# Performance work log

Hardware: AMD Instinct MI355X
Metric: run time of the kernel (lower is better)

## Reference

```python
import jax, jax.numpy as jnp
import numpy as np

D = 8        # input_path_dim (number of driving channels / base vector fields)
N = 256      # cde_state_dim
H = 512      # vf_hidden_dim
B = 4096     # batch of evaluation points (vmapped calls)
P = D * (D - 1) // 2            # number of depth-2 Lyndon brackets (i<j)
M = D + P                       # total brackets = depth-2 Lyndon basis size
_II, _JJ = np.triu_indices(D, k=1)   # Lyndon words (i,j), i<j


def _mlp_fields(h, W1, b1, W2, b2, W3, b3, Wo, bo):
    # eqx.nn.MLP(in=N, out=D*N, width=H, depth=3, softplus hidden, tanh final)
    x = jax.nn.softplus(W1 @ h + b1)
    x = jax.nn.softplus(W2 @ x + b2)
    x = jax.nn.softplus(W3 @ x + b3)
    return jnp.tanh(Wo @ x + bo).reshape(D, N)   # V_i(h), i=1..D


def setup_inputs() -> dict:
    key = jax.random.key(0)
    ks = jax.random.split(key, 10)

    def lin(kw, kb, out_dim, in_dim):
        lim = 1.0 / np.sqrt(in_dim)
        W = jax.random.uniform(kw, (out_dim, in_dim), minval=-lim, maxval=lim, dtype=jnp.float32)
        b = jax.random.uniform(kb, (out_dim,), minval=-lim, maxval=lim, dtype=jnp.float32)
        return W, b

    W1, b1 = lin(ks[0], ks[1], H, N)
    W2, b2 = lin(ks[2], ks[3], H, H)
    W3, b3 = lin(ks[4], ks[5], H, H)
    Wo, bo = lin(ks[6], ks[7], D * N, H)
    h = jax.random.normal(ks[8], (B, N), dtype=jnp.float32)
    primitive_signature = jax.random.normal(ks[9], (B, M), dtype=jnp.float32) * 0.1
    return {
        "h": h, "primitive_signature": primitive_signature,
        "W1": W1, "b1": b1, "W2": W2, "b2": b2,
        "W3": W3, "b3": b3, "Wo": Wo, "bo": bo,
    }


def reference(h, primitive_signature, W1, b1, W2, b2, W3, b3, Wo, bo):
    def single(hv, sig):
        F = lambda y: _mlp_fields(y, W1, b1, W2, b2, W3, b3, Wo, bo)  # [D, N]
        V = F(hv)                                                      # level-1 brackets V_i(h)
        # J[k, i] = DV_i(h) @ V_k(h); one jvp per base-field direction
        J = jax.vmap(lambda v: jax.jvp(F, (hv,), (v,))[1])(V)          # [D, D, N]
        # Lyndon lift, depth 2: [V_i, V_j](h) = DV_j V_i - DV_i V_j, i<j
        lvl2 = J[_II, _JJ] - J[_JJ, _II]                               # [P, N]
        brackets = jnp.concatenate([V, lvl2], axis=0)                  # [M, N]
        # log-ODE contraction against primitive log-signature coefficients
        return jnp.einsum("mn,m->n", brackets, sig)                    # [N]

    return jax.vmap(single)(h, primitive_signature)                    # [B, N]
```

## Files before the change

kernel.cpp:

```cpp
#include <hip/hip_runtime.h>
#include <hip/hip_bf16.h>
#include <math.h>

#define MM 36

typedef _Float16 f16;
typedef __attribute__((ext_vector_type(8))) _Float16 f16x8;
typedef __attribute__((ext_vector_type(4))) _Float16 f16x4;
typedef __attribute__((ext_vector_type(4))) float f32x4;

enum { EPI_NONE = 0, EPI_SPSIG = 1, EPI_TANH = 2, EPI_GATE = 3 };

__device__ __forceinline__ void gl_lds16(const f16* g, f16* l) {
    __builtin_amdgcn_global_load_lds(
        (const __attribute__((address_space(1))) void*)g,
        (__attribute__((address_space(3))) void*)l, 16, 0, 0);
}

template <int EPI, int BM>
__global__ __launch_bounds__(256, 3) void gemm16(
    const f16* __restrict__ A, int lda, long aZ,
    const f16* __restrict__ W, int ldw, long wZ,
    const float* __restrict__ bias,
    void* __restrict__ C0v, int ldc, long cZ,
    f16* __restrict__ C1,
    const f16* __restrict__ G,
    int K, int cshift)
{
    constexpr int WCOLS = (BM == 128) ? 2 : 4;
    constexpr int FN    = (BM == 128) ? 4 : 2;

    __shared__ f16 As[2][BM * 32];
    __shared__ f16 Ws[2][128 * 32];

    const int t = threadIdx.x;
    const int z = blockIdx.z;
    A += (size_t)z * aZ;
    W += (size_t)z * wZ;

    const int nxy = gridDim.x * gridDim.y;
    const int orig = blockIdx.x + gridDim.x * blockIdx.y;
    const int q = nxy >> 3, r = nxy & 7;
    const int xcd = orig & 7, idx = orig >> 3;
    const int nid = (xcd < r ? xcd * (q + 1) : r * (q + 1) + (xcd - r) * q) + idx;
    const long rowTile = (long)(nid >> cshift) * BM;
    const long colTile = (long)(nid & ((1 << cshift) - 1)) * 128;

    const int wave = t >> 6;
    const int lane = t & 63;
    const int wr = (wave / WCOLS) * 64;
    const int wc = (wave % WCOLS) * (FN * 16);
    const int lr = lane & 15;
    const int lk = lane >> 4;

    const int srow = t >> 2;
    const int skq = (t & 3) * 8;
    const f16* Ag = A + (rowTile + srow) * lda + skq;
    const f16* Wg = W + (colTile + srow) * ldw + skq;
    const long lda64 = (long)lda * 64;
    const long ldw64 = (long)ldw * 64;

    f32x4 acc[4][FN];
    const f32x4 zero = {0.f, 0.f, 0.f, 0.f};
#pragma unroll
    for (int m = 0; m < 4; ++m)
#pragma unroll
        for (int n = 0; n < FN; ++n) acc[m][n] = zero;

    const int nt = K >> 5;
    gl_lds16(Ag, &As[0][t * 8]);
    if constexpr (BM == 128) gl_lds16(Ag + lda64, &As[0][(t + 256) * 8]);
    gl_lds16(Wg, &Ws[0][t * 8]);
    gl_lds16(Wg + ldw64, &Ws[0][(t + 256) * 8]);

    for (int ti = 0; ti < nt; ++ti) {
        const int buf = ti & 1;
        __syncthreads();
        if (ti + 1 < nt) {
            const int k0 = (ti + 1) << 5;
            gl_lds16(Ag + k0, &As[buf ^ 1][t * 8]);
            if constexpr (BM == 128) gl_lds16(Ag + k0 + lda64, &As[buf ^ 1][(t + 256) * 8]);
            gl_lds16(Wg + k0, &Ws[buf ^ 1][t * 8]);
            gl_lds16(Wg + k0 + ldw64, &Ws[buf ^ 1][(t + 256) * 8]);
        }
        f16x8 a[4], b[FN];
#pragma unroll
        for (int m = 0; m < 4; ++m)
            a[m] = *(const f16x8*)&As[buf][(wr + m * 16 + lr) * 32 + lk * 8];
#pragma unroll
        for (int n = 0; n < FN; ++n)
            b[n] = *(const f16x8*)&Ws[buf][(wc + n * 16 + lr) * 32 + lk * 8];
#pragma unroll
        for (int m = 0; m < 4; ++m)
#pragma unroll
            for (int n = 0; n < FN; ++n)
                acc[m][n] = __builtin_amdgcn_mfma_f32_16x16x32_f16(a[m], b[n], acc[m][n], 0, 0, 0);
    }

    const long row0 = rowTile + wr + lk * 4;
    const long col0 = colTile + wc + lr;

#pragma unroll
    for (int m = 0; m < 4; ++m) {
#pragma unroll
        for (int n = 0; n < FN; ++n) {
            const long col = col0 + n * 16;
            const float bb = bias ? bias[col] : 0.f;
#pragma unroll
            for (int j = 0; j < 4; ++j) {
                const long row = row0 + m * 16 + j;
                const float x = acc[m][n][j] + bb;
                if constexpr (EPI == EPI_SPSIG) {
                    const float e = __expf(-fabsf(x));
                    const float r1 = __builtin_amdgcn_rcpf(1.f + e);
                    const float sp = fmaxf(x, 0.f) + __logf(1.f + e);
                    const float sg = (x >= 0.f) ? r1 : e * r1;
                    f16* S = (f16*)C0v;
                    S[row * ldc + col] = (f16)sp;
                    C1[row * ldc + col] = (f16)sg;
                } else if constexpr (EPI == EPI_TANH) {
                    const float e2 = __expf(2.f * x);
                    const float th = 1.f - 2.f * __builtin_amdgcn_rcpf(e2 + 1.f);
                    f16* S = (f16*)C0v;
                    S[row * ldc + col] = (f16)th;
                } else if constexpr (EPI == EPI_GATE) {
                    f16* S = (f16*)C0v;
                    const float g = (float)G[(row >> 3) * ldc + col];
                    S[row * ldc + col] = (f16)(x * g);
                } else {
                    float* S = (float*)C0v + (size_t)z * cZ;
                    S[row * ldc + col] = x;
                }
            }
        }
    }
}

__global__ __launch_bounds__(256) void ktilde16(
    const f16* __restrict__ V, const float* __restrict__ sig,
    f16* __restrict__ T, int b0)
{
    const int bl = blockIdx.x * 4 + (threadIdx.x >> 6);
    const int n0 = (threadIdx.x & 63) * 4;
    const f16* vb = V + (size_t)bl * 2048 + n0;
    float v[8][4];
#pragma unroll
    for (int k = 0; k < 8; ++k) {
        const f16x4 x = *(const f16x4*)&vb[k * 256];
#pragma unroll
        for (int j = 0; j < 4; ++j) v[k][j] = (float)x[j];
    }
    const float* sg = sig + (size_t)(b0 + bl) * MM + 8;
    float s2[28];
#pragma unroll
    for (int p = 0; p < 28; ++p) s2[p] = sg[p];

    f16* tb = T + (size_t)bl * 2048 + n0;
#pragma unroll
    for (int i = 0; i < 8; ++i) {
        float a0 = 0.f, a1 = 0.f, a2 = 0.f, a3 = 0.f;
#pragma unroll
        for (int k = 0; k < 8; ++k) {
            if (k == i) continue;
            const int a = (k < i) ? k : i;
            const int b = (k < i) ? i : k;
            const int p = a * (15 - a) / 2 + (b - a - 1);
            const float c = (k < i) ? s2[p] : -s2[p];
            a0 = fmaf(c, v[k][0], a0); a1 = fmaf(c, v[k][1], a1);
            a2 = fmaf(c, v[k][2], a2); a3 = fmaf(c, v[k][3], a3);
        }
        f16x4 o;
        o[0] = (f16)a0; o[1] = (f16)a1; o[2] = (f16)a2; o[3] = (f16)a3;
        *(f16x4*)&tb[i * 256] = o;
    }
}

__global__ __launch_bounds__(256) void finish16(
    const f16* __restrict__ V, const float* __restrict__ Oi,
    const float* __restrict__ sig, float* __restrict__ out, int b0, int C)
{
    const int bl = blockIdx.x * 4 + (threadIdx.x >> 6);
    const int n0 = (threadIdx.x & 63) * 4;
    const float* sg = sig + (size_t)(b0 + bl) * MM;
    float a0 = 0.f, a1 = 0.f, a2 = 0.f, a3 = 0.f;
#pragma unroll
    for (int i = 0; i < 8; ++i) {
        const f16x4 vv = *(const f16x4*)&V[(size_t)bl * 2048 + i * 256 + n0];
        const float4 o = *(const float4*)&Oi[((size_t)i * C + bl) * 256 + n0];
        const float s = sg[i];
        const float v0 = (float)vv[0], v1 = (float)vv[1];
        const float v2 = (float)vv[2], v3 = (float)vv[3];
        a0 = fmaf(s, v0, a0); a0 = fmaf(1.f - v0 * v0, o.x, a0);
        a1 = fmaf(s, v1, a1); a1 = fmaf(1.f - v1 * v1, o.y, a1);
        a2 = fmaf(s, v2, a2); a2 = fmaf(1.f - v2 * v2, o.z, a2);
        a3 = fmaf(s, v3, a3); a3 = fmaf(1.f - v3 * v3, o.w, a3);
    }
    float4 ov; ov.x = a0; ov.y = a1; ov.z = a2; ov.w = a3;
    *(float4*)&out[(size_t)(b0 + bl) * 256 + n0] = ov;
}

__global__ __launch_bounds__(256) void cvt16(
    const float* __restrict__ x, f16* __restrict__ y, int n)
{
    const int i = (blockIdx.x * 256 + threadIdx.x) * 4;
    if (i < n) {
        const float4 v = *(const float4*)&x[i];
        f16x4 o;
        o[0] = (f16)v.x; o[1] = (f16)v.y; o[2] = (f16)v.z; o[3] = (f16)v.w;
        *(f16x4*)&y[i] = o;
    }
}

extern "C" void kernel_launch(void* const* d_in, const int* in_sizes, int n_in,
                              void* d_out, int out_size, void* d_ws, size_t ws_size,
                              hipStream_t stream) {
    const float* h   = (const float*)d_in[0];
    const float* sig = (const float*)d_in[1];
    const float* W1  = (const float*)d_in[2];
    const float* b1  = (const float*)d_in[3];
    const float* W2  = (const float*)d_in[4];
    const float* b2  = (const float*)d_in[5];
    const float* W3  = (const float*)d_in[6];
    const float* b3  = (const float*)d_in[7];
    const float* Wo  = (const float*)d_in[8];
    const float* bo  = (const float*)d_in[9];
    float* out = (float*)d_out;

    char* p = (char*)d_ws;
    f16* W1h = (f16*)p; p += (size_t)512 * 256 * 2;
    f16* W2h = (f16*)p; p += (size_t)512 * 512 * 2;
    f16* W3h = (f16*)p; p += (size_t)512 * 512 * 2;
    f16* Woh = (f16*)p; p += (size_t)2048 * 512 * 2;
    const size_t fixed = (size_t)(p - (char*)d_ws);

    int C = 4096;
    while (C > 128 && fixed + (size_t)C * 31232 > ws_size) C >>= 1;

    f16* h16 = (f16*)p; p += (size_t)C * 256 * 2;
    f16* s1 = (f16*)p;  p += (size_t)C * 512 * 2;
    f16* g1 = (f16*)p;  p += (size_t)C * 512 * 2;
    f16* s2 = (f16*)p;  p += (size_t)C * 512 * 2;
    f16* g2 = (f16*)p;  p += (size_t)C * 512 * 2;
    f16* s3 = (f16*)p;  p += (size_t)C * 512 * 2;
    f16* g3 = (f16*)p;  p += (size_t)C * 512 * 2;
    f16* V  = (f16*)p;  p += (size_t)C * 2048 * 2;
    f16* T  = (f16*)p;  p += (size_t)C * 2048 * 2;
    f16* Ua = (f16*)p;  p += (size_t)C * 4096 * 2;
    f16* Ub = (f16*)p;
    float* Oi = (float*)Ub;

    const dim3 blk(256);
    cvt16<<<dim3(512 * 256 / 1024), blk, 0, stream>>>(W1, W1h, 512 * 256);
    cvt16<<<dim3(512 * 512 / 1024), blk, 0, stream>>>(W2, W2h, 512 * 512);
    cvt16<<<dim3(512 * 512 / 1024), blk, 0, stream>>>(W3, W3h, 512 * 512);
    cvt16<<<dim3(2048 * 512 / 1024), blk, 0, stream>>>(Wo, Woh, 2048 * 512);

    for (int b0 = 0; b0 < 4096; b0 += C) {
        cvt16<<<dim3(C * 256 / 1024), blk, 0, stream>>>(h + (size_t)b0 * 256, h16, C * 256);
        gemm16<EPI_SPSIG, 64><<<dim3(4, C / 64), blk, 0, stream>>>(
            h16, 256, 0, W1h, 256, 0, b1, s1, 512, 0, g1, nullptr, 256, 2);
        gemm16<EPI_SPSIG, 64><<<dim3(4, C / 64), blk, 0, stream>>>(
            s1, 512, 0, W2h, 512, 0, b2, s2, 512, 0, g2, nullptr, 512, 2);
        gemm16<EPI_SPSIG, 64><<<dim3(4, C / 64), blk, 0, stream>>>(
            s2, 512, 0, W3h, 512, 0, b3, s3, 512, 0, g3, nullptr, 512, 2);
        gemm16<EPI_TANH, 128><<<dim3(16, C / 128), blk, 0, stream>>>(
            s3, 512, 0, Woh, 512, 0, bo, V, 2048, 0, nullptr, nullptr, 512, 4);
        ktilde16<<<dim3(C / 4), blk, 0, stream>>>(V, sig, T, b0);
        gemm16<EPI_GATE, 128><<<dim3(4, C / 16), blk, 0, stream>>>(
            T, 256, 0, W1h, 256, 0, nullptr, Ua, 512, 0, nullptr, g1, 256, 2);
        gemm16<EPI_GATE, 128><<<dim3(4, C / 16), blk, 0, stream>>>(
            Ua, 512, 0, W2h, 512, 0, nullptr, Ub, 512, 0, nullptr, g2, 512, 2);
        gemm16<EPI_GATE, 128><<<dim3(4, C / 16), blk, 0, stream>>>(
            Ub, 512, 0, W3h, 512, 0, nullptr, Ua, 512, 0, nullptr, g3, 512, 2);
        gemm16<EPI_NONE, 128><<<dim3(2, C / 128, 8), blk, 0, stream>>>(
            Ua, 4096, 512, Woh, 512, (long)256 * 512, nullptr, Oi, 256, (long)C * 256,
            nullptr, nullptr, 512, 1);
        finish16<<<dim3(C / 4), blk, 0, stream>>>(V, Oi, sig, out, b0, C);
    }
}
```

Measured before the change: 186.5 us.

## Generalize GEMM tiling, use 512-thread 256-row tiles, fp16 Oi, fuse weight casts

Templates the GEMM on tile sizes, thread count and wave layout, and switches the output and tangent GEMMs to 256x128 tiles run by 512 threads. The goal is more operand reuse per staged tile. The final per-channel GEMM now stores its result in fp16 instead of fp32, which halves that traffic but costs some precision. The four weight-conversion launches are merged into one kernel. The larger tiles need more LDS and registers per block, which may limit occupancy.

```diff
diff --git a/kernel.cpp b/kernel.cpp
--- a/kernel.cpp
+++ b/kernel.cpp
@@ -17,8 +17,8 @@
         (__attribute__((address_space(3))) void*)l, 16, 0, 0);
 }
 
-template <int EPI, int BM>
-__global__ __launch_bounds__(256, 3) void gemm16(
+template <int EPI, int BM, int BN, int TPB, int WN>
+__global__ __launch_bounds__(TPB, (TPB == 512) ? 6 : 3) void gemm16(
     const f16* __restrict__ A, int lda, long aZ,
     const f16* __restrict__ W, int ldw, long wZ,
     const float* __restrict__ bias,
@@ -27,11 +27,14 @@
     const f16* __restrict__ G,
     int K, int cshift)
 {
-    constexpr int WCOLS = (BM == 128) ? 2 : 4;
-    constexpr int FN    = (BM == 128) ? 4 : 2;
+    constexpr int WM = TPB / 64 / WN;
+    constexpr int FM = BM / (WM * 16);
+    constexpr int FN = BN / (WN * 16);
+    constexpr int LA = BM * 4 / TPB;
+    constexpr int LB = BN * 4 / TPB;
 
     __shared__ f16 As[2][BM * 32];
-    __shared__ f16 Ws[2][128 * 32];
+    __shared__ f16 Ws[2][BN * 32];
 
     const int t = threadIdx.x;
     const int z = blockIdx.z;
@@ -44,54 +47,51 @@
     const int xcd = orig & 7, idx = orig >> 3;
     const int nid = (xcd < r ? xcd * (q + 1) : r * (q + 1) + (xcd - r) * q) + idx;
     const long rowTile = (long)(nid >> cshift) * BM;
-    const long colTile = (long)(nid & ((1 << cshift) - 1)) * 128;
+    const long colTile = (long)(nid & ((1 << cshift) - 1)) * BN;
 
     const int wave = t >> 6;
     const int lane = t & 63;
-    const int wr = (wave / WCOLS) * 64;
-    const int wc = (wave % WCOLS) * (FN * 16);
+    const int wr = (wave / WN) * (FM * 16);
+    const int wc = (wave % WN) * (FN * 16);
     const int lr = lane & 15;
     const int lk = lane >> 4;
 
-    const int srow = t >> 2;
-    const int skq = (t & 3) * 8;
-    const f16* Ag = A + (rowTile + srow) * lda + skq;
-    const f16* Wg = W + (colTile + srow) * ldw + skq;
-    const long lda64 = (long)lda * 64;
-    const long ldw64 = (long)ldw * 64;
-
-    f32x4 acc[4][FN];
+    const f16* Ag = A + (rowTile + (t >> 2)) * lda + (t & 3) * 8;
+    const f16* Wg = W + (colTile + (t >> 2)) * ldw + (t & 3) * 8;
+
+    f32x4 acc[FM][FN];
     const f32x4 zero = {0.f, 0.f, 0.f, 0.f};
 #pragma unroll
-    for (int m = 0; m < 4; ++m)
+    for (int m = 0; m < FM; ++m)
 #pragma unroll
         for (int n = 0; n < FN; ++n) acc[m][n] = zero;
 
     const int nt = K >> 5;
-    gl_lds16(Ag, &As[0][t * 8]);
-    if constexpr (BM == 128) gl_lds16(Ag + lda64, &As[0][(t + 256) * 8]);
-    gl_lds16(Wg, &Ws[0][t * 8]);
-    gl_lds16(Wg + ldw64, &Ws[0][(t + 256) * 8]);
+
+    auto stage = [&](int buf, int k0) {
+#pragma unroll
+        for (int p = 0; p < LA; ++p)
+            gl_lds16(Ag + (long)p * (TPB / 4) * lda + k0, &As[buf][(p * TPB + t) * 8]);
+#pragma unroll
+        for (int p = 0; p < LB; ++p)
+            gl_lds16(Wg + (long)p * (TPB / 4) * ldw + k0, &Ws[buf][(p * TPB + t) * 8]);
+    };
+
+    stage(0, 0);
 
     for (int ti = 0; ti < nt; ++ti) {
         const int buf = ti & 1;
         __syncthreads();
-        if (ti + 1 < nt) {
-            const int k0 = (ti + 1) << 5;
-            gl_lds16(Ag + k0, &As[buf ^ 1][t * 8]);
-            if constexpr (BM == 128) gl_lds16(Ag + k0 + lda64, &As[buf ^ 1][(t + 256) * 8]);
-            gl_lds16(Wg + k0, &Ws[buf ^ 1][t * 8]);
-            gl_lds16(Wg + k0 + ldw64, &Ws[buf ^ 1][(t + 256) * 8]);
-        }
-        f16x8 a[4], b[FN];
-#pragma unroll
-        for (int m = 0; m < 4; ++m)
+        if (ti + 1 < nt) stage(buf ^ 1, (ti + 1) << 5);
+        f16x8 a[FM], b[FN];
+#pragma unroll
+        for (int m = 0; m < FM; ++m)
             a[m] = *(const f16x8*)&As[buf][(wr + m * 16 + lr) * 32 + lk * 8];
 #pragma unroll
         for (int n = 0; n < FN; ++n)
             b[n] = *(const f16x8*)&Ws[buf][(wc + n * 16 + lr) * 32 + lk * 8];
 #pragma unroll
-        for (int m = 0; m < 4; ++m)
+        for (int m = 0; m < FM; ++m)
 #pragma unroll
             for (int n = 0; n < FN; ++n)
                 acc[m][n] = __builtin_amdgcn_mfma_f32_16x16x32_f16(a[m], b[n], acc[m][n], 0, 0, 0);
@@ -101,7 +101,7 @@
     const long col0 = colTile + wc + lr;
 
 #pragma unroll
-    for (int m = 0; m < 4; ++m) {
+    for (int m = 0; m < FM; ++m) {
 #pragma unroll
         for (int n = 0; n < FN; ++n) {
             const long col = col0 + n * 16;
@@ -128,8 +128,8 @@
                     const float g = (float)G[(row >> 3) * ldc + col];
                     S[row * ldc + col] = (f16)(x * g);
                 } else {
-                    float* S = (float*)C0v + (size_t)z * cZ;
-                    S[row * ldc + col] = x;
+                    f16* S = (f16*)C0v + (size_t)z * cZ;
+                    S[row * ldc + col] = (f16)x;
                 }
             }
         }
@@ -176,7 +176,7 @@
 }
 
 __global__ __launch_bounds__(256) void finish16(
-    const f16* __restrict__ V, const float* __restrict__ Oi,
+    const f16* __restrict__ V, const f16* __restrict__ Oi,
     const float* __restrict__ sig, float* __restrict__ out, int b0, int C)
 {
     const int bl = blockIdx.x * 4 + (threadIdx.x >> 6);
@@ -186,17 +186,36 @@
 #pragma unroll
     for (int i = 0; i < 8; ++i) {
         const f16x4 vv = *(const f16x4*)&V[(size_t)bl * 2048 + i * 256 + n0];
-        const float4 o = *(const float4*)&Oi[((size_t)i * C + bl) * 256 + n0];
+        const f16x4 oo = *(const f16x4*)&Oi[((size_t)i * C + bl) * 256 + n0];
         const float s = sg[i];
         const float v0 = (float)vv[0], v1 = (float)vv[1];
         const float v2 = (float)vv[2], v3 = (float)vv[3];
-        a0 = fmaf(s, v0, a0); a0 = fmaf(1.f - v0 * v0, o.x, a0);
-        a1 = fmaf(s, v1, a1); a1 = fmaf(1.f - v1 * v1, o.y, a1);
-        a2 = fmaf(s, v2, a2); a2 = fmaf(1.f - v2 * v2, o.z, a2);
-        a3 = fmaf(s, v3, a3); a3 = fmaf(1.f - v3 * v3, o.w, a3);
+        a0 = fmaf(s, v0, a0); a0 = fmaf(1.f - v0 * v0, (float)oo[0], a0);
+        a1 = fmaf(s, v1, a1); a1 = fmaf(1.f - v1 * v1, (float)oo[1], a1);
+        a2 = fmaf(s, v2, a2); a2 = fmaf(1.f - v2 * v2, (float)oo[2], a2);
+        a3 = fmaf(s, v3, a3); a3 = fmaf(1.f - v3 * v3, (float)oo[3], a3);
     }
     float4 ov; ov.x = a0; ov.y = a1; ov.z = a2; ov.w = a3;
     *(float4*)&out[(size_t)(b0 + bl) * 256 + n0] = ov;
+}
+
+__global__ __launch_bounds__(256) void cvtW(
+    const float* __restrict__ W1, const float* __restrict__ W2,
+    const float* __restrict__ W3, const float* __restrict__ Wo,
+    f16* __restrict__ o1, f16* __restrict__ o2,
+    f16* __restrict__ o3, f16* __restrict__ oo)
+{
+    long i = (long)blockIdx.x * 256 + threadIdx.x;
+    const float* src; f16* dst; long base;
+    if (i < 32768)       { src = W1; dst = o1; base = 0; }
+    else if (i < 98304)  { src = W2; dst = o2; base = 32768; }
+    else if (i < 163840) { src = W3; dst = o3; base = 98304; }
+    else                 { src = Wo; dst = oo; base = 163840; }
+    i -= base;
+    const float4 v = ((const float4*)src)[i];
+    f16x4 o;
+    o[0] = (f16)v.x; o[1] = (f16)v.y; o[2] = (f16)v.z; o[3] = (f16)v.w;
+    ((f16x4*)dst)[i] = o;
 }
 
 __global__ __launch_bounds__(256) void cvt16(
@@ -247,32 +266,30 @@
     f16* T  = (f16*)p;  p += (size_t)C * 2048 * 2;
     f16* Ua = (f16*)p;  p += (size_t)C * 4096 * 2;
     f16* Ub = (f16*)p;
-    float* Oi = (float*)Ub;
+    f16* Oi = Ub;
 
     const dim3 blk(256);
-    cvt16<<<dim3(512 * 256 / 1024), blk, 0, stream>>>(W1, W1h, 512 * 256);
-    cvt16<<<dim3(512 * 512 / 1024), blk, 0, stream>>>(W2, W2h, 512 * 512);
-    cvt16<<<dim3(512 * 512 / 1024), blk, 0, stream>>>(W3, W3h, 512 * 512);
-    cvt16<<<dim3(2048 * 512 / 1024), blk, 0, stream>>>(Wo, Woh, 2048 * 512);
+    const dim3 blk5(512);
+    cvtW<<<dim3(1664), blk, 0, stream>>>(W1, W2, W3, Wo, W1h, W2h, W3h, Woh);
 
     for (int b0 = 0; b0 < 4096; b0 += C) {
         cvt16<<<dim3(C * 256 / 1024), blk, 0, stream>>>(h + (size_t)b0 * 256, h16, C * 256);
-        gemm16<EPI_SPSIG, 64><<<dim3(4, C / 64), blk, 0, stream>>>(
+        gemm16<EPI_SPSIG, 64, 128, 256, 4><<<dim3(4, C / 64), blk, 0, stream>>>(
             h16, 256, 0, W1h, 256, 0, b1, s1, 512, 0, g1, nullptr, 256, 2);
-        gemm16<EPI_SPSIG, 64><<<dim3(4, C / 64), blk, 0, stream>>>(
+        gemm16<EPI_SPSIG, 64, 128, 256, 4><<<dim3(4, C / 64), blk, 0, stream>>>(
             s1, 512, 0, W2h, 512, 0, b2, s2, 512, 0, g2, nullptr, 512, 2);
-        gemm16<EPI_SPSIG, 64><<<dim3(4, C / 64), blk, 0, stream>>>(
+        gemm16<EPI_SPSIG, 64, 128, 256, 4><<<dim3(4, C / 64), blk, 0, stream>>>(
             s2, 512, 0, W3h, 512, 0, b3, s3, 512, 0, g3, nullptr, 512, 2);
-        gemm16<EPI_TANH, 128><<<dim3(16, C / 128), blk, 0, stream>>>(
+        gemm16<EPI_TANH, 256, 128, 512, 2><<<dim3(16, C / 256), blk5, 0, stream>>>(
             s3, 512, 0, Woh, 512, 0, bo, V, 2048, 0, nullptr, nullptr, 512, 4);
         ktilde16<<<dim3(C / 4), blk, 0, stream>>>(V, sig, T, b0);
-        gemm16<EPI_GATE, 128><<<dim3(4, C / 16), blk, 0, stream>>>(
+        gemm16<EPI_GATE, 256, 128, 512, 2><<<dim3(4, C / 32), blk5, 0, stream>>>(
             T, 256, 0, W1h, 256, 0, nullptr, Ua, 512, 0, nullptr, g1, 256, 2);
-        gemm16<EPI_GATE, 128><<<dim3(4, C / 16), blk, 0, stream>>>(
+        gemm16<EPI_GATE, 256, 128, 512, 2><<<dim3(4, C / 32), blk5, 0, stream>>>(
             Ua, 512, 0, W2h, 512, 0, nullptr, Ub, 512, 0, nullptr, g2, 512, 2);
-        gemm16<EPI_GATE, 128><<<dim3(4, C / 16), blk, 0, stream>>>(
+        gemm16<EPI_GATE, 256, 128, 512, 2><<<dim3(4, C / 32), blk5, 0, stream>>>(
             Ub, 512, 0, W3h, 512, 0, nullptr, Ua, 512, 0, nullptr, g3, 512, 2);
-        gemm16<EPI_NONE, 128><<<dim3(2, C / 128, 8), blk, 0, stream>>>(
+        gemm16<EPI_NONE, 128, 128, 256, 2><<<dim3(2, C / 128, 8), blk, 0, stream>>>(
             Ua, 4096, 512, Woh, 512, (long)256 * 512, nullptr, Oi, 256, (long)C * 256,
             nullptr, nullptr, 512, 1);
         finish16<<<dim3(C / 4), blk, 0, stream>>>(V, Oi, sig, out, b0, C);
```

Result: slower. 385.8 us (+106.9%).
